# Kernel optimization log

Hardware: AMD Instinct MI355X
Metric: run time of the kernel (lower is better)

The kernel has to match this reference:

```python
import jax, jax.numpy as jnp
import numpy as np

ALPHA = 0.1
NUM_SAMPLES = 4096
EPS = 1e-12
B, D_IN, D_OUT = 4096, 32768, 128


def setup_inputs() -> dict:
    key = jax.random.key(0)
    k_x, k_mu, k_eps = jax.random.split(key, 3)
    x = jax.random.normal(k_x, (B, D_IN), dtype=jnp.float32)
    weight_mu = jax.random.normal(k_mu, (D_OUT, D_IN), dtype=jnp.float32) * 0.01
    sigma1 = jnp.full((D_OUT, D_IN), 0.5, dtype=jnp.float32)      # posterior std param
    spike1 = jnp.full((D_OUT, D_IN), ALPHA, dtype=jnp.float32)    # init uniform(alpha, alpha)
    prior_sig = jnp.full((D_OUT, D_IN), 0.5, dtype=jnp.float32)   # prior std buffer
    eps_noise = jax.random.normal(k_eps, (B, D_OUT), dtype=jnp.float32)
    return {"x": x, "weight_mu": weight_mu, "sigma1": sigma1,
            "spike1": spike1, "prior_sig": prior_sig, "eps_noise": eps_noise}


def _forward(x, weight_mu, sigma1, spike1, prior_sig, eps_noise):
    # sig1 = clamp(relu(sigma1), min=eps); spike = clamp(spike1, 1e-6, 1-1e-6)
    sig1 = jnp.maximum(jax.nn.relu(sigma1), EPS)
    spike = jnp.clip(spike1, 1e-6, 1.0 - 1e-6)

    # local reparameterization: mean/var of pre-activations under spike-slab posterior
    mean_pre = spike * weight_mu                                   # [D_out, D_in]
    var_pre = spike * sig1 ** 2 + spike * weight_mu ** 2 - mean_pre ** 2

    m = x @ mean_pre.T                                             # [B, D_out]
    v = (x ** 2) @ var_pre.T                                       # [B, D_out]
    s = eps_noise * jnp.sqrt(v)
    out = jnp.stack((m + s, m - s), axis=0)                        # [2, B, D_out]

    # KL divergence between spike-slab posterior and prior
    prior_var = prior_sig ** 2
    log_prior_var = jnp.log(prior_var)
    logvar = jnp.log(sig1 ** 2)
    kl_gauss = -0.5 * jnp.sum(spike * (1.0 + logvar - log_prior_var
                                       - weight_mu ** 2 / prior_var
                                       - jnp.exp(logvar) / prior_var))
    kl_spike = jnp.sum((1.0 - spike) * jnp.log((1.0 - spike) / (1.0 - ALPHA))
                       + spike * jnp.log(spike / ALPHA))
    kl = (kl_gauss + kl_spike) / NUM_SAMPLES
    return out, kl


def reference(x, weight_mu, sigma1, spike1, prior_sig, eps_noise):
    return _forward(x, weight_mu, sigma1, spike1, prior_sig, eps_noise)
```

## Files before the change

kernel.cpp:

```cpp
#include <hip/hip_runtime.h>

#define D_IN 32768
#define D_OUT 128
#define NB 4096
#define NKC 8
#define KC (D_IN / NKC)
#define BM 128
#define BK 64
#define NSTEP (KC / BK)

typedef __bf16 bf16x8 __attribute__((ext_vector_type(8)));
typedef __bf16 bf16x4 __attribute__((ext_vector_type(4)));
typedef float f32x4 __attribute__((ext_vector_type(4)));

__device__ __forceinline__ int swz(int r, int c) {
  return r * BK + (c ^ ((r & 7) << 3));
}

__global__ void prep_kernel(const float* __restrict__ mu, const float* __restrict__ sg,
                            const float* __restrict__ sp, const float* __restrict__ pg,
                            __bf16* __restrict__ wcomb, float* __restrict__ kl_acc) {
  const int NV = D_OUT * D_IN / 4;
  float kl = 0.f;
  for (int i = blockIdx.x * blockDim.x + threadIdx.x; i < NV; i += gridDim.x * blockDim.x) {
    const int e = i * 4;
    const int r = e >> 15;
    const int c = e & (D_IN - 1);
    const float4 m4 = *(const float4*)(mu + e);
    const float4 s4 = *(const float4*)(sg + e);
    const float4 p4 = *(const float4*)(sp + e);
    const float4 g4 = *(const float4*)(pg + e);
    const float mv[4] = {m4.x, m4.y, m4.z, m4.w};
    const float sv[4] = {s4.x, s4.y, s4.z, s4.w};
    const float pv4[4] = {p4.x, p4.y, p4.z, p4.w};
    const float gv[4] = {g4.x, g4.y, g4.z, g4.w};
    bf16x4 mo, vo;
#pragma unroll
    for (int j = 0; j < 4; ++j) {
      const float m_ = mv[j];
      const float s_ = fmaxf(sv[j], 1e-12f);
      const float p_ = fminf(fmaxf(pv4[j], 1e-6f), 1.f - 1e-6f);
      const float pvar = gv[j] * gv[j];
      const float mean = p_ * m_;
      const float var = p_ * s_ * s_ + p_ * (1.f - p_) * m_ * m_;
      mo[j] = (__bf16)mean;
      vo[j] = (__bf16)var;
      const float rr = (s_ * s_) / pvar;
      kl += -0.5f * p_ * (1.f + __logf(rr) - (m_ * m_) / pvar - rr);
      kl += (1.f - p_) * __logf((1.f - p_) * (1.f / 0.9f)) + p_ * __logf(p_ * 10.f);
    }
    *(bf16x4*)(wcomb + (size_t)r * D_IN + c) = mo;
    *(bf16x4*)(wcomb + (size_t)(D_OUT + r) * D_IN + c) = vo;
  }
#pragma unroll
  for (int off = 32; off > 0; off >>= 1) kl += __shfl_down(kl, off);
  __shared__ float red[4];
  const int lane = threadIdx.x & 63;
  const int wid = threadIdx.x >> 6;
  if (lane == 0) red[wid] = kl;
  __syncthreads();
  if (threadIdx.x == 0) atomicAdd(kl_acc, red[0] + red[1] + red[2] + red[3]);
}

__global__ __launch_bounds__(1024, 4) void gemm_kernel(const float* __restrict__ x,
                                                       const __bf16* __restrict__ wcomb,
                                                       float* __restrict__ partial) {
  __shared__ __bf16 lds[2][32768];

  const int bid = blockIdx.x;
  const int kc = bid & (NKC - 1);
  const int mb = bid >> 3;
  const int m0 = mb * BM;
  const size_t k0 = (size_t)kc * KC;

  const int t = threadIdx.x;
  const int lane = t & 63;
  const int wid = t >> 6;
  const int wm = wid >> 2;
  const int wn = wid & 3;

  const int xrow = t >> 3;
  const int xc = (t & 7) << 3;
  const int wrow = t >> 2;
  const int wc = (t & 3) << 4;

  const float* xg = x + (size_t)xrow * D_IN + k0 + xc;
  const __bf16* wg = wcomb + (size_t)wrow * D_IN + k0 + wc;

  const int xoff = swz(xrow, xc);
  const int woff0 = 16384 + swz(wrow, wc);
  const int woff1 = 16384 + swz(wrow, wc + 8);

  f32x4 acc[2][4];
#pragma unroll
  for (int i = 0; i < 2; ++i)
#pragma unroll
    for (int j = 0; j < 4; ++j) acc[i][j] = (f32x4){0.f, 0.f, 0.f, 0.f};

  const int l15 = lane & 15;
  const int lk = (lane >> 4) << 3;
  const int abase = (wn >= 2) ? 8192 : 0;
  const int ar0 = wm * 32 + l15;
  const int br0 = wn * 64 + l15;

  float4 xr0 = *(const float4*)(xg);
  float4 xr1 = *(const float4*)(xg + 4);
  uint4 wr0 = *(const uint4*)(wg);
  uint4 wr1 = *(const uint4*)(wg + 8);

  for (int i = 0; i < NSTEP; ++i) {
    __bf16* buf = lds[i & 1];

    {
      const float vv[8] = {xr0.x, xr0.y, xr0.z, xr0.w, xr1.x, xr1.y, xr1.z, xr1.w};
      bf16x8 a, s;
#pragma unroll
      for (int j = 0; j < 8; ++j) {
        const float f = vv[j];
        a[j] = (__bf16)f;
        s[j] = (__bf16)(f * f);
      }
      *(bf16x8*)(buf + xoff) = a;
      *(bf16x8*)(buf + 8192 + xoff) = s;
      *(uint4*)(buf + woff0) = wr0;
      *(uint4*)(buf + woff1) = wr1;
    }

    if (i + 1 < NSTEP) {
      const int kn = (i + 1) * BK;
      xr0 = *(const float4*)(xg + kn);
      xr1 = *(const float4*)(xg + kn + 4);
      wr0 = *(const uint4*)(wg + kn);
      wr1 = *(const uint4*)(wg + kn + 8);
    }

    asm volatile("s_waitcnt lgkmcnt(0)" ::: "memory");
    __builtin_amdgcn_s_barrier();

#pragma unroll
    for (int kk = 0; kk < 2; ++kk) {
      const int col = kk * 32 + lk;
      bf16x8 af[2], bfv[4];
#pragma unroll
      for (int mi = 0; mi < 2; ++mi)
        af[mi] = *(const bf16x8*)(buf + abase + swz(ar0 + mi * 16, col));
#pragma unroll
      for (int ni = 0; ni < 4; ++ni)
        bfv[ni] = *(const bf16x8*)(buf + 16384 + swz(br0 + ni * 16, col));
#pragma unroll
      for (int mi = 0; mi < 2; ++mi)
#pragma unroll
        for (int ni = 0; ni < 4; ++ni)
          acc[mi][ni] = __builtin_amdgcn_mfma_f32_16x16x32_bf16(af[mi], bfv[ni],
                                                                acc[mi][ni], 0, 0, 0);
    }
  }

  float* pp = partial + (size_t)kc * ((size_t)NB * 2 * D_OUT);
  const int crow = (lane >> 4) << 2;
  const int ccol = lane & 15;
#pragma unroll
  for (int mi = 0; mi < 2; ++mi) {
    const int grow = m0 + wm * 32 + mi * 16 + crow;
#pragma unroll
    for (int ni = 0; ni < 4; ++ni) {
      const int gcol = wn * 64 + ni * 16 + ccol;
      const f32x4 a = acc[mi][ni];
#pragma unroll
      for (int j = 0; j < 4; ++j)
        pp[(size_t)(grow + j) * (2 * D_OUT) + gcol] = a[j];
    }
  }
}

__global__ void reduce_kernel(const float* __restrict__ partial,
                              const float* __restrict__ eps,
                              const float* __restrict__ kl_acc,
                              float* __restrict__ out) {
  const int tid = blockIdx.x * blockDim.x + threadIdx.x;
  if (tid == 0) out[2 * NB * D_OUT] = kl_acc[0] * (1.0f / 4096.0f);
  if (tid >= NB * D_OUT / 4) return;
  const int b = tid >> 5;
  const int j = (tid & 31) << 2;
  float m[4] = {0.f, 0.f, 0.f, 0.f}, v[4] = {0.f, 0.f, 0.f, 0.f};
#pragma unroll
  for (int q = 0; q < NKC; ++q) {
    const float* p = partial + ((size_t)q * NB + b) * (2 * D_OUT);
    const float4 mm = *(const float4*)(p + j);
    const float4 vv = *(const float4*)(p + D_OUT + j);
    m[0] += mm.x; m[1] += mm.y; m[2] += mm.z; m[3] += mm.w;
    v[0] += vv.x; v[1] += vv.y; v[2] += vv.z; v[3] += vv.w;
  }
  const float4 e4 = *(const float4*)(eps + (size_t)b * D_OUT + j);
  const float ev[4] = {e4.x, e4.y, e4.z, e4.w};
  float4 o0, o1;
  float* o0p = (float*)&o0;
  float* o1p = (float*)&o1;
#pragma unroll
  for (int jj = 0; jj < 4; ++jj) {
    const float s = ev[jj] * sqrtf(fmaxf(v[jj], 0.f));
    o0p[jj] = m[jj] + s;
    o1p[jj] = m[jj] - s;
  }
  *(float4*)(out + (size_t)b * D_OUT + j) = o0;
  *(float4*)(out + (size_t)NB * D_OUT + (size_t)b * D_OUT + j) = o1;
}

extern "C" void kernel_launch(void* const* d_in, const int* in_sizes, int n_in,
                              void* d_out, int out_size, void* d_ws, size_t ws_size,
                              hipStream_t stream) {
  const float* x   = (const float*)d_in[0];
  const float* mu  = (const float*)d_in[1];
  const float* sg  = (const float*)d_in[2];
  const float* sp  = (const float*)d_in[3];
  const float* pg  = (const float*)d_in[4];
  const float* eps = (const float*)d_in[5];
  float* out = (float*)d_out;

  __bf16* wcomb = (__bf16*)d_ws;
  float* partial = (float*)((char*)d_ws + (size_t)16 * 1024 * 1024);
  float* kl_acc = (float*)((char*)d_ws + (size_t)48 * 1024 * 1024);

  hipMemsetAsync(kl_acc, 0, sizeof(float), stream);
  prep_kernel<<<2048, 256, 0, stream>>>(mu, sg, sp, pg, wcomb, kl_acc);
  gemm_kernel<<<(NB / BM) * NKC, 1024, 0, stream>>>(x, wcomb, partial);
  reduce_kernel<<<(NB * D_OUT / 4) / 256, 256, 0, stream>>>(partial, eps, kl_acc, out);
}
```

Baseline: 129.1 us.

## Store split-K partials in fp16 and replace KL atomic/memset with per-block partials

The GEMM now writes its split-K partial sums as fp16 instead of fp32, halving partial-buffer write and read traffic between the GEMM and the reduce kernel. The KL reduction drops the memset and global atomic: each prep block writes its own partial and block 0 of the reduce kernel sums them, which removes one launch. The cost is precision, since fp16 partials can lose accuracy or overflow on large pre-activation values.

```diff
diff --git a/kernel.cpp b/kernel.cpp
--- a/kernel.cpp
+++ b/kernel.cpp
@@ -8,10 +8,12 @@
 #define BM 128
 #define BK 64
 #define NSTEP (KC / BK)
+#define PREP_BLOCKS 2048
 
 typedef __bf16 bf16x8 __attribute__((ext_vector_type(8)));
 typedef __bf16 bf16x4 __attribute__((ext_vector_type(4)));
 typedef float f32x4 __attribute__((ext_vector_type(4)));
+typedef _Float16 half4 __attribute__((ext_vector_type(4)));
 
 __device__ __forceinline__ int swz(int r, int c) {
   return r * BK + (c ^ ((r & 7) << 3));
@@ -19,7 +21,7 @@
 
 __global__ void prep_kernel(const float* __restrict__ mu, const float* __restrict__ sg,
                             const float* __restrict__ sp, const float* __restrict__ pg,
-                            __bf16* __restrict__ wcomb, float* __restrict__ kl_acc) {
+                            __bf16* __restrict__ wcomb, float* __restrict__ kl_part) {
   const int NV = D_OUT * D_IN / 4;
   float kl = 0.f;
   for (int i = blockIdx.x * blockDim.x + threadIdx.x; i < NV; i += gridDim.x * blockDim.x) {
@@ -59,12 +61,12 @@
   const int wid = threadIdx.x >> 6;
   if (lane == 0) red[wid] = kl;
   __syncthreads();
-  if (threadIdx.x == 0) atomicAdd(kl_acc, red[0] + red[1] + red[2] + red[3]);
+  if (threadIdx.x == 0) kl_part[blockIdx.x] = red[0] + red[1] + red[2] + red[3];
 }
 
 __global__ __launch_bounds__(1024, 4) void gemm_kernel(const float* __restrict__ x,
                                                        const __bf16* __restrict__ wcomb,
-                                                       float* __restrict__ partial) {
+                                                       _Float16* __restrict__ partial) {
   __shared__ __bf16 lds[2][32768];
 
   const int bid = blockIdx.x;
@@ -156,7 +158,7 @@
     }
   }
 
-  float* pp = partial + (size_t)kc * ((size_t)NB * 2 * D_OUT);
+  _Float16* pp = partial + (size_t)kc * ((size_t)NB * 2 * D_OUT);
   const int crow = (lane >> 4) << 2;
   const int ccol = lane & 15;
 #pragma unroll
@@ -168,42 +170,58 @@
       const f32x4 a = acc[mi][ni];
 #pragma unroll
       for (int j = 0; j < 4; ++j)
-        pp[(size_t)(grow + j) * (2 * D_OUT) + gcol] = a[j];
-    }
-  }
-}
-
-__global__ void reduce_kernel(const float* __restrict__ partial,
+        pp[(size_t)(grow + j) * (2 * D_OUT) + gcol] = (_Float16)a[j];
+    }
+  }
+}
+
+__global__ void reduce_kernel(const _Float16* __restrict__ partial,
                               const float* __restrict__ eps,
-                              const float* __restrict__ kl_acc,
+                              const float* __restrict__ kl_part,
                               float* __restrict__ out) {
   const int tid = blockIdx.x * blockDim.x + threadIdx.x;
-  if (tid == 0) out[2 * NB * D_OUT] = kl_acc[0] * (1.0f / 4096.0f);
-  if (tid >= NB * D_OUT / 4) return;
-  const int b = tid >> 5;
-  const int j = (tid & 31) << 2;
-  float m[4] = {0.f, 0.f, 0.f, 0.f}, v[4] = {0.f, 0.f, 0.f, 0.f};
-#pragma unroll
-  for (int q = 0; q < NKC; ++q) {
-    const float* p = partial + ((size_t)q * NB + b) * (2 * D_OUT);
-    const float4 mm = *(const float4*)(p + j);
-    const float4 vv = *(const float4*)(p + D_OUT + j);
-    m[0] += mm.x; m[1] += mm.y; m[2] += mm.z; m[3] += mm.w;
-    v[0] += vv.x; v[1] += vv.y; v[2] += vv.z; v[3] += vv.w;
-  }
-  const float4 e4 = *(const float4*)(eps + (size_t)b * D_OUT + j);
-  const float ev[4] = {e4.x, e4.y, e4.z, e4.w};
-  float4 o0, o1;
-  float* o0p = (float*)&o0;
-  float* o1p = (float*)&o1;
-#pragma unroll
-  for (int jj = 0; jj < 4; ++jj) {
-    const float s = ev[jj] * sqrtf(fmaxf(v[jj], 0.f));
-    o0p[jj] = m[jj] + s;
-    o1p[jj] = m[jj] - s;
-  }
-  *(float4*)(out + (size_t)b * D_OUT + j) = o0;
-  *(float4*)(out + (size_t)NB * D_OUT + (size_t)b * D_OUT + j) = o1;
+  if (tid < NB * D_OUT / 4) {
+    const int b = tid >> 5;
+    const int j = (tid & 31) << 2;
+    float m[4] = {0.f, 0.f, 0.f, 0.f}, v[4] = {0.f, 0.f, 0.f, 0.f};
+#pragma unroll
+    for (int q = 0; q < NKC; ++q) {
+      const _Float16* p = partial + ((size_t)q * NB + b) * (2 * D_OUT);
+      const half4 mm = *(const half4*)(p + j);
+      const half4 vv = *(const half4*)(p + D_OUT + j);
+#pragma unroll
+      for (int k = 0; k < 4; ++k) {
+        m[k] += (float)mm[k];
+        v[k] += (float)vv[k];
+      }
+    }
+    const float4 e4 = *(const float4*)(eps + (size_t)b * D_OUT + j);
+    const float ev[4] = {e4.x, e4.y, e4.z, e4.w};
+    float4 o0, o1;
+    float* o0p = (float*)&o0;
+    float* o1p = (float*)&o1;
+#pragma unroll
+    for (int jj = 0; jj < 4; ++jj) {
+      const float s = ev[jj] * sqrtf(fmaxf(v[jj], 0.f));
+      o0p[jj] = m[jj] + s;
+      o1p[jj] = m[jj] - s;
+    }
+    *(float4*)(out + (size_t)b * D_OUT + j) = o0;
+    *(float4*)(out + (size_t)NB * D_OUT + (size_t)b * D_OUT + j) = o1;
+  }
+  if (blockIdx.x == 0) {
+    float kl = 0.f;
+    for (int i = threadIdx.x; i < PREP_BLOCKS; i += 256) kl += kl_part[i];
+#pragma unroll
+    for (int off = 32; off > 0; off >>= 1) kl += __shfl_down(kl, off);
+    __shared__ float red[4];
+    const int lane = threadIdx.x & 63;
+    const int wid = threadIdx.x >> 6;
+    if (lane == 0) red[wid] = kl;
+    __syncthreads();
+    if (threadIdx.x == 0)
+      out[2 * NB * D_OUT] = (red[0] + red[1] + red[2] + red[3]) * (1.0f / 4096.0f);
+  }
 }
 
 extern "C" void kernel_launch(void* const* d_in, const int* in_sizes, int n_in,
@@ -218,11 +236,10 @@
   float* out = (float*)d_out;
 
   __bf16* wcomb = (__bf16*)d_ws;
-  float* partial = (float*)((char*)d_ws + (size_t)16 * 1024 * 1024);
-  float* kl_acc = (float*)((char*)d_ws + (size_t)48 * 1024 * 1024);
-
-  hipMemsetAsync(kl_acc, 0, sizeof(float), stream);
-  prep_kernel<<<2048, 256, 0, stream>>>(mu, sg, sp, pg, wcomb, kl_acc);
+  _Float16* partial = (_Float16*)((char*)d_ws + (size_t)16 * 1024 * 1024);
+  float* kl_part = (float*)((char*)d_ws + (size_t)32 * 1024 * 1024);
+
+  prep_kernel<<<PREP_BLOCKS, 256, 0, stream>>>(mu, sg, sp, pg, wcomb, kl_part);
   gemm_kernel<<<(NB / BM) * NKC, 1024, 0, stream>>>(x, wcomb, partial);
-  reduce_kernel<<<(NB * D_OUT / 4) / 256, 256, 0, stream>>>(partial, eps, kl_acc, out);
-}
+  reduce_kernel<<<(NB * D_OUT / 4) / 256, 256, 0, stream>>>(partial, eps, kl_part, out);
+}
```

After: 104.3 us. 19.2% less time.
